# Optimization experiments

Measured on AMD Instinct MI355X. Metric: run time of the kernel, lower is better.

The kernel has to match this reference:

```python
import jax, jax.numpy as jnp
import numpy as np

BITS = 4
PACK = 32 // BITS  # 8 nibbles per int32
MASK = (1 << BITS) - 1  # 0xF, maxq for 4-bit


def _unpack_rows(q):
    # q: [K//PACK, N] int32, nibbles packed along the input (row) dim
    shifts = (jnp.arange(PACK, dtype=jnp.int32) * BITS)
    vals = (q[:, None, :] >> shifts[None, :, None]) & MASK  # [K//PACK, PACK, N]
    return vals.reshape(q.shape[0] * PACK, q.shape[1])      # [K, N]


def _unpack_cols(q):
    # q: [1, N//PACK] int32, nibbles packed along the output (col) dim
    shifts = (jnp.arange(PACK, dtype=jnp.int32) * BITS)
    vals = (q[:, :, None] >> shifts[None, None, :]) & MASK  # [1, N//PACK, PACK]
    return vals.reshape(q.shape[0], q.shape[1] * PACK)       # [1, N]


def setup_inputs() -> dict:
    key = jax.random.key(0)
    k1, k2, k3, k4 = jax.random.split(key, 4)
    M, K, N = 4096, 4096, 11008
    x = jax.random.normal(k1, (M, K), dtype=jnp.float16)
    qweight = jax.random.randint(k2, (K // PACK, N), jnp.iinfo(jnp.int32).min,
                                 jnp.iinfo(jnp.int32).max, dtype=jnp.int32)
    qzeros = jax.random.randint(k3, (1, N // PACK), jnp.iinfo(jnp.int32).min,
                                jnp.iinfo(jnp.int32).max, dtype=jnp.int32)
    # realistic small positive per-channel scales
    scales = (jax.random.uniform(k4, (1, N), dtype=jnp.float32) * 0.01 + 1e-3).astype(jnp.float16)
    return {"x": x, "qweight": qweight, "qzeros": qzeros, "scales": scales}


def reference(x, qweight, qzeros, scales):
    # GPTQ/exllama 4-bit dequant: w = scale * (q - (zero + 1)), single group
    wq = _unpack_rows(qweight)                      # [K, N] int32 in [0, 15]
    zeros = _unpack_cols(qzeros) + 1                # [1, N] int32
    w = (wq - zeros).astype(jnp.float16) * scales   # [K, N] fp16
    out = jnp.dot(x, w)                             # [M, N] fp16 GEMM
    return out
```

## Files before the change

kernel.cpp:

```cpp
#include <hip/hip_runtime.h>
#include <stdint.h>

#define M_DIM 4096
#define K_DIM 4096
#define N_DIM 11008

typedef _Float16 half2v __attribute__((ext_vector_type(2)));
typedef _Float16 half8  __attribute__((ext_vector_type(8)));
typedef float    f32x4  __attribute__((ext_vector_type(4)));

__device__ __forceinline__ unsigned int pkrtz_bits(float a, float b) {
  typedef __fp16 fp16x2 __attribute__((ext_vector_type(2)));
  union { fp16x2 h; unsigned int u; } c;
  c.h = __builtin_amdgcn_cvt_pkrtz(a, b);
  return c.u;
}

__device__ __forceinline__ half8 pack8(float4 lo, float4 hi) {
  union { unsigned int u[4]; half8 v; } r;
  r.u[0] = pkrtz_bits(lo.x, hi.x);
  r.u[1] = pkrtz_bits(lo.y, hi.y);
  r.u[2] = pkrtz_bits(lo.z, hi.z);
  r.u[3] = pkrtz_bits(lo.w, hi.w);
  return r.v;
}

__global__ __launch_bounds__(256) void convert_x(const float* __restrict__ X,
                                                 _Float16* __restrict__ X16) {
  size_t g = (size_t)blockIdx.x * 256 + threadIdx.x;
  const float4* p = (const float4*)(X + g * 8);
  float4 lo = p[0], hi = p[1];
  *(half8*)(X16 + g * 8) = pack8(lo, hi);
}

__device__ __forceinline__ half8 unpack8(unsigned int q, half2v zoff) {
  union { unsigned int u; half2v h; } t0, t1, t2, t3;
  t0.u = (q & 0x000F000Fu) | 0x64006400u;
  t1.u = ((q >> 4) & 0x000F000Fu) | 0x64006400u;
  t2.u = ((q >> 8) & 0x000F000Fu) | 0x64006400u;
  t3.u = ((q >> 12) & 0x000F000Fu) | 0x64006400u;
  union { half2v h[4]; half8 v; } r;
  r.h[0] = t0.h - zoff;
  r.h[1] = t1.h - zoff;
  r.h[2] = t2.h - zoff;
  r.h[3] = t3.h - zoff;
  return r.v;
}

template <bool PRE>
__global__ __launch_bounds__(256, 3) void gptq_gemm(
    const float* __restrict__ X32,
    const _Float16* __restrict__ X16,
    const int* __restrict__ QW,
    const int* __restrict__ QZ,
    const float* __restrict__ SC,
    float* __restrict__ OUT) {
  const int tid  = threadIdx.x;
  const int lane = tid & 63;
  const int wave = tid >> 6;
  const int quad = lane >> 4;
  const int l16  = lane & 15;
  const int bx = blockIdx.x;
  const int by = blockIdx.y;

  __shared__ half8 ldsA[512];

  const int mrow = by * 128 + (tid & 127);
  const half8*  gx16 = PRE ? (const half8*)(X16 + (size_t)mrow * K_DIM) + (tid >> 7) : nullptr;
  const float4* gx32 = !PRE ? (const float4*)(X32 + (size_t)mrow * K_DIM) + (tid >> 7) * 2 : nullptr;

  const int* qp = QW + (size_t)quad * N_DIM + bx * 128 + wave * 32 + l16;

  half2v zoff[2];
  float sc[2];
#pragma unroll
  for (int nt = 0; nt < 2; ++nt) {
    int n = bx * 128 + wave * 32 + nt * 16 + l16;
    int z = (QZ[n >> 3] >> ((n & 7) * 4)) & 15;
    union { unsigned int u; half2v h; } zc;
    unsigned int zb = 0x6400u + (unsigned int)(z + 1);
    zc.u = (zb << 16) | zb;
    zoff[nt] = zc.h;
    sc[nt] = SC[n];
  }

  f32x4 acc[8][2] = {};

  half8 va = {}, vb = {};
  float4 f0 = {}, f1 = {}, f2 = {}, f3 = {};
  if (PRE) { va = gx16[0]; vb = gx16[2]; }
  else     { f0 = gx32[0]; f1 = gx32[1]; f2 = gx32[4]; f3 = gx32[5]; }
  int q0 = qp[0], q1 = qp[16];

  for (int ks = 0; ks < 128; ++ks) {
    __syncthreads();
    if (PRE) {
      ldsA[tid]       = va;
      ldsA[tid + 256] = vb;
    } else {
      ldsA[tid]       = pack8(f0, f1);
      ldsA[tid + 256] = pack8(f2, f3);
    }

    half8 nva = va, nvb = vb;
    float4 nf0 = f0, nf1 = f1, nf2 = f2, nf3 = f3;
    int nq0 = q0, nq1 = q1;
    if (ks < 127) {
      qp += 4 * N_DIM;
      nq0 = qp[0]; nq1 = qp[16];
      if (PRE) { gx16 += 4; nva = gx16[0]; nvb = gx16[2]; }
      else     { gx32 += 8; nf0 = gx32[0]; nf1 = gx32[1]; nf2 = gx32[4]; nf3 = gx32[5]; }
    }
    __syncthreads();

    half8 b0 = unpack8((unsigned int)q0, zoff[0]);
    half8 b1 = unpack8((unsigned int)q1, zoff[1]);
#pragma unroll
    for (int mt = 0; mt < 8; ++mt) {
      half8 a = ldsA[quad * 128 + mt * 16 + l16];
      acc[mt][0] = __builtin_amdgcn_mfma_f32_16x16x32_f16(a, b0, acc[mt][0], 0, 0, 0);
      acc[mt][1] = __builtin_amdgcn_mfma_f32_16x16x32_f16(a, b1, acc[mt][1], 0, 0, 0);
    }

    va = nva; vb = nvb;
    f0 = nf0; f1 = nf1; f2 = nf2; f3 = nf3;
    q0 = nq0; q1 = nq1;
  }

#pragma unroll
  for (int mt = 0; mt < 8; ++mt) {
    int mbase = by * 128 + mt * 16 + quad * 4;
#pragma unroll
    for (int nt = 0; nt < 2; ++nt) {
      int n = bx * 128 + wave * 32 + nt * 16 + l16;
      float s = sc[nt];
#pragma unroll
      for (int p = 0; p < 4; ++p) {
        OUT[(size_t)(mbase + p) * N_DIM + n] = acc[mt][nt][p] * s;
      }
    }
  }
}

extern "C" void kernel_launch(void* const* d_in, const int* in_sizes, int n_in,
                              void* d_out, int out_size, void* d_ws, size_t ws_size,
                              hipStream_t stream) {
  const float* X  = (const float*)d_in[0];
  const int* QW   = (const int*)d_in[1];
  const int* QZ   = (const int*)d_in[2];
  const float* SC = (const float*)d_in[3];
  float* OUT      = (float*)d_out;

  dim3 grid(N_DIM / 128, M_DIM / 128);
  const size_t x16_bytes = (size_t)M_DIM * K_DIM * sizeof(_Float16);

  if (ws_size >= x16_bytes) {
    _Float16* X16 = (_Float16*)d_ws;
    convert_x<<<dim3((M_DIM * (size_t)K_DIM / 8) / 256), 256, 0, stream>>>(X, X16);
    gptq_gemm<true><<<grid, 256, 0, stream>>>(X, X16, QW, QZ, SC, OUT);
  } else {
    gptq_gemm<false><<<grid, 256, 0, stream>>>(X, nullptr, QW, QZ, SC, OUT);
  }
}
```

Measured before the change: 796.8 us.

## Use 2x2 wave tiling with double-buffered direct global-to-LDS A staging

Restructures the GEMM so each wave computes a 64x64 sub-tile (4x4 MFMA tiles) instead of 128x32, which raises register-level reuse of A fragments and dequantized B. The A tile is staged with global_load_lds directly into a double-buffered LDS array with a K step of 64, so there is one barrier per step. The fp32 fallback path is removed and the workspace conversion is assumed to always be available. The costs are more LDS, more accumulator registers, and a dependence on ws_size being large enough.

```diff
diff --git a/kernel.cpp b/kernel.cpp
--- a/kernel.cpp
+++ b/kernel.cpp
@@ -47,9 +47,13 @@
   return r.v;
 }
 
-template <bool PRE>
+__device__ __forceinline__ void stage16(const void* g, void* l) {
+  __builtin_amdgcn_global_load_lds((__attribute__((address_space(1))) unsigned int*)g,
+                                   (__attribute__((address_space(3))) unsigned int*)l,
+                                   16, 0, 0);
+}
+
 __global__ __launch_bounds__(256, 3) void gptq_gemm(
-    const float* __restrict__ X32,
     const _Float16* __restrict__ X16,
     const int* __restrict__ QW,
     const int* __restrict__ QZ,
@@ -58,24 +62,25 @@
   const int tid  = threadIdx.x;
   const int lane = tid & 63;
   const int wave = tid >> 6;
+  const int wr   = wave >> 1;
+  const int wc   = wave & 1;
   const int quad = lane >> 4;
   const int l16  = lane & 15;
   const int bx = blockIdx.x;
   const int by = blockIdx.y;
 
-  __shared__ half8 ldsA[512];
+  __shared__ __align__(16) _Float16 ldsA[2 * 1024 * 8];
 
-  const int mrow = by * 128 + (tid & 127);
-  const half8*  gx16 = PRE ? (const half8*)(X16 + (size_t)mrow * K_DIM) + (tid >> 7) : nullptr;
-  const float4* gx32 = !PRE ? (const float4*)(X32 + (size_t)mrow * K_DIM) + (tid >> 7) * 2 : nullptr;
+  const _Float16* gA = X16 + (size_t)(by * 128 + (tid & 127)) * K_DIM + (tid >> 7) * 8;
+  _Float16* lA = ldsA + (size_t)tid * 8;
 
-  const int* qp = QW + (size_t)quad * N_DIM + bx * 128 + wave * 32 + l16;
+  const int* qp = QW + (size_t)quad * N_DIM + bx * 128 + wc * 64 + l16;
 
-  half2v zoff[2];
-  float sc[2];
+  half2v zoff[4];
+  float sc[4];
 #pragma unroll
-  for (int nt = 0; nt < 2; ++nt) {
-    int n = bx * 128 + wave * 32 + nt * 16 + l16;
+  for (int nt = 0; nt < 4; ++nt) {
+    int n = bx * 128 + wc * 64 + nt * 16 + l16;
     int z = (QZ[n >> 3] >> ((n & 7) * 4)) & 15;
     union { unsigned int u; half2v h; } zc;
     unsigned int zb = 0x6400u + (unsigned int)(z + 1);
@@ -84,60 +89,74 @@
     sc[nt] = SC[n];
   }
 
-  f32x4 acc[8][2] = {};
+  f32x4 acc[4][4] = {};
 
-  half8 va = {}, vb = {};
-  float4 f0 = {}, f1 = {}, f2 = {}, f3 = {};
-  if (PRE) { va = gx16[0]; vb = gx16[2]; }
-  else     { f0 = gx32[0]; f1 = gx32[1]; f2 = gx32[4]; f3 = gx32[5]; }
-  int q0 = qp[0], q1 = qp[16];
+#pragma unroll
+  for (int i = 0; i < 4; ++i)
+    stage16(gA + i * 16, lA + i * 2048);
+  int q[2][4];
+#pragma unroll
+  for (int s = 0; s < 2; ++s)
+#pragma unroll
+    for (int nt = 0; nt < 4; ++nt)
+      q[s][nt] = qp[(s * 4) * N_DIM + nt * 16];
+  __syncthreads();
 
-  for (int ks = 0; ks < 128; ++ks) {
-    __syncthreads();
-    if (PRE) {
-      ldsA[tid]       = va;
-      ldsA[tid + 256] = vb;
-    } else {
-      ldsA[tid]       = pack8(f0, f1);
-      ldsA[tid + 256] = pack8(f2, f3);
+  int p = 0;
+  for (int ks = 0; ks < 64; ++ks) {
+    int nq[2][4];
+    if (ks < 63) {
+      gA += 64;
+      qp += 8 * N_DIM;
+      _Float16* lb = ldsA + (p ^ 1) * 8192 + (size_t)tid * 8;
+#pragma unroll
+      for (int i = 0; i < 4; ++i)
+        stage16(gA + i * 16, lb + i * 2048);
+#pragma unroll
+      for (int s = 0; s < 2; ++s)
+#pragma unroll
+        for (int nt = 0; nt < 4; ++nt)
+          nq[s][nt] = qp[(s * 4) * N_DIM + nt * 16];
     }
 
-    half8 nva = va, nvb = vb;
-    float4 nf0 = f0, nf1 = f1, nf2 = f2, nf3 = f3;
-    int nq0 = q0, nq1 = q1;
-    if (ks < 127) {
-      qp += 4 * N_DIM;
-      nq0 = qp[0]; nq1 = qp[16];
-      if (PRE) { gx16 += 4; nva = gx16[0]; nvb = gx16[2]; }
-      else     { gx32 += 8; nf0 = gx32[0]; nf1 = gx32[1]; nf2 = gx32[4]; nf3 = gx32[5]; }
+    const _Float16* base = ldsA + p * 8192;
+#pragma unroll
+    for (int s = 0; s < 2; ++s) {
+      half8 a[4];
+#pragma unroll
+      for (int mt = 0; mt < 4; ++mt)
+        a[mt] = *(const half8*)(base + ((s * 4 + quad) * 128 + wr * 64 + mt * 16 + l16) * 8);
+      half8 b[4];
+#pragma unroll
+      for (int nt = 0; nt < 4; ++nt)
+        b[nt] = unpack8((unsigned int)q[s][nt], zoff[nt]);
+#pragma unroll
+      for (int mt = 0; mt < 4; ++mt)
+#pragma unroll
+        for (int nt = 0; nt < 4; ++nt)
+          acc[mt][nt] = __builtin_amdgcn_mfma_f32_16x16x32_f16(a[mt], b[nt], acc[mt][nt], 0, 0, 0);
     }
     __syncthreads();
-
-    half8 b0 = unpack8((unsigned int)q0, zoff[0]);
-    half8 b1 = unpack8((unsigned int)q1, zoff[1]);
+    if (ks < 63) {
 #pragma unroll
-    for (int mt = 0; mt < 8; ++mt) {
-      half8 a = ldsA[quad * 128 + mt * 16 + l16];
-      acc[mt][0] = __builtin_amdgcn_mfma_f32_16x16x32_f16(a, b0, acc[mt][0], 0, 0, 0);
-      acc[mt][1] = __builtin_amdgcn_mfma_f32_16x16x32_f16(a, b1, acc[mt][1], 0, 0, 0);
+      for (int s = 0; s < 2; ++s)
+#pragma unroll
+        for (int nt = 0; nt < 4; ++nt)
+          q[s][nt] = nq[s][nt];
     }
-
-    va = nva; vb = nvb;
-    f0 = nf0; f1 = nf1; f2 = nf2; f3 = nf3;
-    q0 = nq0; q1 = nq1;
+    p ^= 1;
   }
 
 #pragma unroll
-  for (int mt = 0; mt < 8; ++mt) {
-    int mbase = by * 128 + mt * 16 + quad * 4;
+  for (int mt = 0; mt < 4; ++mt) {
+    int mbase = by * 128 + wr * 64 + mt * 16 + quad * 4;
 #pragma unroll
-    for (int nt = 0; nt < 2; ++nt) {
-      int n = bx * 128 + wave * 32 + nt * 16 + l16;
+    for (int nt = 0; nt < 4; ++nt) {
+      int n = bx * 128 + wc * 64 + nt * 16 + l16;
       float s = sc[nt];
 #pragma unroll
-      for (int p = 0; p < 4; ++p) {
-        OUT[(size_t)(mbase + p) * N_DIM + n] = acc[mt][nt][p] * s;
-      }
+      for (int pp = 0; pp < 4; ++pp)
+        OUT[(size_t)(mbase + pp) * N_DIM + n] = acc[mt][nt][pp] * s;
     }
   }
 }
@@ -150,15 +169,9 @@
   const int* QZ   = (const int*)d_in[2];
   const float* SC = (const float*)d_in[3];
   float* OUT      = (float*)d_out;
+  _Float16* X16   = (_Float16*)d_ws;
 
+  convert_x<<<dim3((M_DIM * (size_t)K_DIM / 8) / 256), 256, 0, stream>>>(X, X16);
   dim3 grid(N_DIM / 128, M_DIM / 128);
-  const size_t x16_bytes = (size_t)M_DIM * K_DIM * sizeof(_Float16);
-
-  if (ws_size >= x16_bytes) {
-    _Float16* X16 = (_Float16*)d_ws;
-    convert_x<<<dim3((M_DIM * (size_t)K_DIM / 8) / 256), 256, 0, stream>>>(X, X16);
-    gptq_gemm<true><<<grid, 256, 0, stream>>>(X, X16, QW, QZ, SC, OUT);
-  } else {
-    gptq_gemm<false><<<grid, 256, 0, stream>>>(X, nullptr, QW, QZ, SC, OUT);
-  }
+  gptq_gemm<<<grid, 256, 0, stream>>>(X16, QW, QZ, SC, OUT);
 }
```

Measured after the change: 659.5 us. -17.2%, faster.
